# Performance work log

Hardware: AMD Instinct MI355X
Metric: run time of the kernel (lower is better)

## Reference

```python
import jax, jax.numpy as jnp
import numpy as np


def lstm_step(x_t, h, c, Wih, Whh, bih, bhh):
    # PyTorch LSTM gate order: i, f, g, o
    gates = x_t @ Wih.T + h @ Whh.T + bih + bhh
    i, f, g, o = jnp.split(gates, 4, axis=-1)
    i = jax.nn.sigmoid(i)
    f = jax.nn.sigmoid(f)
    g = jnp.tanh(g)
    o = jax.nn.sigmoid(o)
    c_new = f * c + i * g
    h_new = o * jnp.tanh(c_new)
    return h_new, c_new


def setup_inputs() -> dict:
    key = jax.random.key(0)
    N, C, T, V, M = 512, 3, 300, 25, 2
    F = C * V * M  # 150
    H = 100
    ks = jax.random.split(key, 12)
    s = 1.0 / np.sqrt(H)  # PyTorch LSTM/Linear init scale
    u = lambda k, shape: jax.random.uniform(k, shape, jnp.float32, -s, s)
    return {
        "x": jax.random.normal(ks[0], (N, C, T, V, M), jnp.float32),
        "enc_Wih": u(ks[1], (4 * H, F)),
        "enc_Whh": u(ks[2], (4 * H, H)),
        "enc_bih": u(ks[3], (4 * H,)),
        "enc_bhh": u(ks[4], (4 * H,)),
        "dec_Wih": u(ks[5], (4 * H, F)),
        "dec_Whh": u(ks[6], (4 * H, H)),
        "dec_bih": u(ks[7], (4 * H,)),
        "dec_bhh": u(ks[8], (4 * H,)),
        "fc_W": u(ks[9], (F, H)),
        "fc_b": u(ks[10], (F,)),
    }


def reference(x, enc_Wih, enc_Whh, enc_bih, enc_bhh,
              dec_Wih, dec_Whh, dec_bih, dec_bhh, fc_W, fc_b):
    N, C, T, V, M = x.shape
    F = C * V * M
    H = enc_Whh.shape[1]
    # (N,C,T,V,M) -> (N,T,C*V*M)
    xs = jnp.transpose(x, (0, 2, 1, 3, 4)).reshape(N, T, F)

    # Encoder LSTM: only need final (h, c)
    h0 = jnp.zeros((N, H), x.dtype)
    c0 = jnp.zeros((N, H), x.dtype)

    def enc_step(carry, xt):
        h, c = carry
        h, c = lstm_step(xt, h, c, enc_Wih, enc_Whh, enc_bih, enc_bhh)
        return (h, c), None

    (h, c), _ = jax.lax.scan(enc_step, (h0, c0), jnp.swapaxes(xs, 0, 1))

    inp0 = jnp.zeros((N, F), x.dtype)

    def dec_step(carry, _):
        inp, h, c = carry
        h, c = lstm_step(inp, h, c, dec_Wih, dec_Whh, dec_bih, dec_bhh)
        out = h @ fc_W.T + fc_b
        return (out, h, c), out

    _, outs = jax.lax.scan(dec_step, (inp0, h, c), None, length=T - 1)  # [T-1,N,F]

    # outputs[:,0,:] stays zero, like the torch.zeros buffer
    outputs = jnp.concatenate([jnp.zeros((1, N, F), x.dtype), outs], axis=0)  # [T,N,F]
    outputs = jnp.swapaxes(outputs, 0, 1).reshape(N, T, C, V, M)
    return jnp.transpose(outputs, (0, 2, 1, 3, 4))  # (N,C,T,V,M)
```

## Files before the change

### kernel.cpp

```cpp
#include <hip/hip_runtime.h>
#include <hip/hip_fp16.h>


#define B_W2P   0u
#define B_WDP   102400u
#define B_WEP   204800u
#define B_PIH   307200u
#define B_BENC  460800u
#define B_B1    462848u
#define B_BEFF  464896u
#define B_HIST  466944u
#define HIST_STRIDE 29952
#define B_XG    31137792u

typedef _Float16 h2_t __attribute__((ext_vector_type(2)));

#if defined(__has_builtin)
#if __has_builtin(__builtin_amdgcn_fdot2)
#define HAS_FDOT2 1
#endif
#endif

__device__ __forceinline__ float fdot2u(unsigned a, unsigned b, float c) {
#ifdef HAS_FDOT2
  return __builtin_amdgcn_fdot2(__builtin_bit_cast(h2_t, a), __builtin_bit_cast(h2_t, b), c, false);
#else
  float al = __half2float(__ushort_as_half((unsigned short)(a & 0xffffu)));
  float ah = __half2float(__ushort_as_half((unsigned short)(a >> 16)));
  float bl = __half2float(__ushort_as_half((unsigned short)(b & 0xffffu)));
  float bh = __half2float(__ushort_as_half((unsigned short)(b >> 16)));
  return fmaf(ah, bh, fmaf(al, bl, c));
#endif
}

__device__ __forceinline__ unsigned pack2f(float a, float b) {
  return (unsigned)__half_as_ushort(__float2half(a)) |
         ((unsigned)__half_as_ushort(__float2half(b)) << 16);
}

__device__ __forceinline__ float fast_sig(float x) {
  float e = __builtin_amdgcn_exp2f(x * -1.442695040888963f);
  return __builtin_amdgcn_rcpf(1.f + e);
}
__device__ __forceinline__ float fast_tanh(float x) {
  float e = __builtin_amdgcn_exp2f(x * -2.885390081777926f);
  return fmaf(2.f, __builtin_amdgcn_rcpf(1.f + e), -1.f);
}

__device__ __forceinline__ float lstm_tail(float acc, int ty, float& c) {
  float sg = fast_sig(acc);
  float th = fast_tanh(acc);
  float act = (ty == 2) ? th : sg;
  float v1 = __shfl_xor(act, 1);
  float v2 = __shfl_xor(act, 2);
  float v3 = __shfl_xor(v1, 2);
  c = fmaf(v1, c, act * v2);
  return v3 * fast_tanh(c);
}

__device__ __forceinline__ float dot100(const unsigned short* hb, const unsigned* wp) {
  const uint4* h4 = (const uint4*)hb;
  float a0 = 0.f, a1 = 0.f, a2 = 0.f, a3 = 0.f;
#pragma unroll
  for (int ch = 0; ch < 12; ++ch) {
    uint4 v = h4[ch];
    a0 = fdot2u(wp[4 * ch + 0], v.x, a0);
    a1 = fdot2u(wp[4 * ch + 1], v.y, a1);
    a2 = fdot2u(wp[4 * ch + 2], v.z, a2);
    a3 = fdot2u(wp[4 * ch + 3], v.w, a3);
  }
  uint2 v2 = *(const uint2*)(hb + 96);
  a0 = fdot2u(wp[48], v2.x, a0);
  a1 = fdot2u(wp[49], v2.y, a1);
  return (a0 + a1) + (a2 + a3);
}

__global__ void prep(const float* __restrict__ dWih, const float* __restrict__ dWhh,
                     const float* __restrict__ dbih, const float* __restrict__ dbhh,
                     const float* __restrict__ eWih, const float* __restrict__ eWhh,
                     const float* __restrict__ ebih, const float* __restrict__ ebhh,
                     const float* __restrict__ fcW,  const float* __restrict__ fcb,
                     char* __restrict__ wsb)
{
  int idx = blockIdx.x * 256 + threadIdx.x;
  if (idx < 25600) {
    int q = idx >> 9, t = idx & 511;
    unsigned w2p = 0, wdp = 0, wep = 0;
    if (t < 400) {
      int r = (t & 3) * 100 + (t >> 2);
      int j0 = 2 * q, j1 = 2 * q + 1;
      float wd0 = dWhh[r * 100 + j0], wd1 = dWhh[r * 100 + j1];
      float we0 = eWhh[r * 100 + j0], we1 = eWhh[r * 100 + j1];
      float s0 = 0.f, s1 = 0.f;
      for (int f = 0; f < 150; ++f) {
        float a = dWih[r * 150 + f];
        s0 = fmaf(a, fcW[f * 100 + j0], s0);
        s1 = fmaf(a, fcW[f * 100 + j1], s1);
      }
      w2p = pack2f(wd0 + s0, wd1 + s1);
      wdp = pack2f(wd0, wd1);
      wep = pack2f(we0, we1);
    }
    ((unsigned*)(wsb + B_W2P))[idx] = w2p;
    ((unsigned*)(wsb + B_WDP))[idx] = wdp;
    ((unsigned*)(wsb + B_WEP))[idx] = wep;
  } else if (idx < 25600 + 38400) {
    int k = idx - 25600; int d = k >> 9, t = k & 511;
    unsigned pk = 0;
    if (t < 400) {
      int r = (t & 3) * 100 + (t >> 2);
      pk = pack2f(eWih[r * 150 + 2 * d], eWih[r * 150 + 2 * d + 1]);
    }
    ((unsigned*)(wsb + B_PIH))[k] = pk;
  } else if (idx < 25600 + 38400 + 512) {
    int t = idx - (25600 + 38400);
    float be = 0.f, b1 = 0.f, bf = 0.f;
    if (t < 400) {
      int r = (t & 3) * 100 + (t >> 2);
      be = ebih[r] + ebhh[r];
      b1 = dbih[r] + dbhh[r];
      float acc = 0.f;
      for (int f = 0; f < 150; ++f) acc = fmaf(dWih[r * 150 + f], fcb[f], acc);
      bf = b1 + acc;
    }
    ((float*)(wsb + B_BENC))[t] = be;
    ((float*)(wsb + B_B1))[t]   = b1;
    ((float*)(wsb + B_BEFF))[t] = bf;
  }
}

__global__ __launch_bounds__(512, 4)
void pre(const float* __restrict__ x, const char* __restrict__ wsb,
         unsigned short* __restrict__ xg, int n0)
{
  const int tid = threadIdx.x;
  const int n = n0 + blockIdx.x;
  __shared__ unsigned short xls[150 * 160];

  unsigned wih[75];
  const unsigned* pih = (const unsigned*)(wsb + B_PIH);
#pragma unroll
  for (int d = 0; d < 75; ++d) wih[d] = pih[(d << 9) + tid];

  const float* xb = x + (size_t)n * 45000;
  unsigned short* xgr = xg + (size_t)blockIdx.x * 120000 + ((tid < 400) ? tid : 0);
  const bool on = tid < 400;

  for (int phase = 0; phase < 2; ++phase) {
    const int tbase = phase * 150;
    if (phase) __syncthreads();
    for (int d = tid; d < 150 * 160; d += 512) {
      int tl = d / 160, f = d - tl * 160;
      float v = 0.f;
      if (f < 150) {
        int c = f / 50, q = f - c * 50;
        v = xb[c * 15000 + (tbase + tl) * 50 + q];
      }
      xls[tl * 160 + f] = __half_as_ushort(__float2half(v));
    }
    __syncthreads();
    if (on) {
      for (int tl = 0; tl < 150; ++tl) {
        const uint4* row = (const uint4*)(xls + tl * 160);
        float a0 = 0.f, a1 = 0.f, a2 = 0.f, a3 = 0.f;
#pragma unroll
        for (int ch = 0; ch < 18; ++ch) {
          uint4 v = row[ch];
          a0 = fdot2u(wih[4 * ch + 0], v.x, a0);
          a1 = fdot2u(wih[4 * ch + 1], v.y, a1);
          a2 = fdot2u(wih[4 * ch + 2], v.z, a2);
          a3 = fdot2u(wih[4 * ch + 3], v.w, a3);
        }
        uint4 v = row[18];
        a0 = fdot2u(wih[72], v.x, a0);
        a1 = fdot2u(wih[73], v.y, a1);
        a2 = fdot2u(wih[74], v.z, a2);
        float a = (a0 + a1) + (a2 + a3);
        xgr[(size_t)(tbase + tl) * 400] = __half_as_ushort(__float2half(a));
      }
    }
  }
}

__global__ __launch_bounds__(512, 4)
void recurrent(const unsigned short* __restrict__ xg, char* __restrict__ wsb, int n0)
{
  const int t  = threadIdx.x;
  const int n  = n0 + blockIdx.x;
  const int j  = t >> 2, ty = t & 3;
  const bool leader = (t < 400) && (ty == 0);
  __shared__ unsigned short hh[2][112];

  const unsigned* WEP = (const unsigned*)(wsb + B_WEP);
  const unsigned* WDP = (const unsigned*)(wsb + B_WDP);
  const unsigned* W2P = (const unsigned*)(wsb + B_W2P);

  unsigned wp[50];
#pragma unroll
  for (int q = 0; q < 50; ++q) wp[q] = WEP[(q << 9) + t];

  const float benc = ((const float*)(wsb + B_BENC))[t];
  const float b1g  = ((const float*)(wsb + B_B1))[t];
  const float beff = ((const float*)(wsb + B_BEFF))[t];
  unsigned short* histn = (unsigned short*)(wsb + B_HIST) + (size_t)n * HIST_STRIDE;
  const unsigned short* xgr = xg + (size_t)blockIdx.x * 120000 + ((t < 400) ? t : 0);
  float c = 0.f;

  unsigned short p1 = xgr[400];
  {
    float acc = benc + __half2float(__ushort_as_half(xgr[0]));
    float hn = lstm_tail(acc, ty, c);
    if (leader) hh[1][j] = __half_as_ushort(__float2half(hn));
    __syncthreads();
  }
  for (int ts = 1; ts < 300; ++ts) {
    const int rd = ts & 1, wr = rd ^ 1;
    unsigned short pn = xgr[(size_t)((ts + 1 < 300) ? ts + 1 : 299) * 400];
    float acc = benc + __half2float(__ushort_as_half(p1)) + dot100(hh[rd], wp);
    float hn = lstm_tail(acc, ty, c);
    if (leader) hh[wr][j] = __half_as_ushort(__float2half(hn));
    __syncthreads();
    p1 = pn;
  }

#pragma unroll
  for (int q = 0; q < 50; ++q) wp[q] = WDP[(q << 9) + t];
  {
    float acc = b1g + dot100(hh[0], wp);
    float hn = lstm_tail(acc, ty, c);
    if (leader) {
      hh[1][j] = __half_as_ushort(__float2half(hn));
      histn[j] = __half_as_ushort(__float2half(hn));
    }
    __syncthreads();
  }
#pragma unroll
  for (int q = 0; q < 50; ++q) wp[q] = W2P[(q << 9) + t];
  for (int s = 2; s <= 299; ++s) {
    const int rd = (299 + s) & 1, wr = rd ^ 1;
    float acc = beff + dot100(hh[rd], wp);
    float hn = lstm_tail(acc, ty, c);
    if (leader) {
      hh[wr][j] = __half_as_ushort(__float2half(hn));
      histn[(s - 1) * 100 + j] = __half_as_ushort(__float2half(hn));
    }
    __syncthreads();
  }
}

__global__ __launch_bounds__(192, 4)
void emit(const char* __restrict__ wsb, const float* __restrict__ fcW,
          const float* __restrict__ fcb, float* __restrict__ out)
{
  const int f = threadIdx.x;
  const int n = blockIdx.x;
  const int z = blockIdx.y;
  __shared__ unsigned short hl[15008];

  const uint4* src = (const uint4*)((const unsigned short*)(wsb + B_HIST) +
                                    (size_t)n * HIST_STRIDE + z * 15000);
  for (int k = f; k < 1875; k += 192) ((uint4*)hl)[k] = src[k];

  const bool on = f < 150;
  unsigned fw[50];
  float bias = 0.f;
  if (on) {
    const float* fp = fcW + f * 100;
#pragma unroll
    for (int q = 0; q < 50; ++q) fw[q] = pack2f(fp[2 * q], fp[2 * q + 1]);
    bias = fcb[f];
  }
  __syncthreads();

  if (!on) return;
  const int cc = f / 50, r = f - cc * 50;
  float* ob = out + (size_t)n * 45000 + cc * 15000 + r;
  if (z == 0) ob[0] = 0.f;
  const int rows = z ? 149 : 150;
  for (int tl = 0; tl < rows; ++tl) {
    const uint4* row = (const uint4*)(hl + tl * 100);
    float a0 = bias, a1 = 0.f, a2 = 0.f, a3 = 0.f;
#pragma unroll
    for (int ch = 0; ch < 12; ++ch) {
      uint4 v = row[ch];
      a0 = fdot2u(fw[4 * ch + 0], v.x, a0);
      a1 = fdot2u(fw[4 * ch + 1], v.y, a1);
      a2 = fdot2u(fw[4 * ch + 2], v.z, a2);
      a3 = fdot2u(fw[4 * ch + 3], v.w, a3);
    }
    uint2 v2 = *(const uint2*)(hl + tl * 100 + 96);
    a0 = fdot2u(fw[48], v2.x, a0);
    a1 = fdot2u(fw[49], v2.y, a1);
    const int tt = z * 150 + tl + 1;
    ob[tt * 50] = (a0 + a1) + (a2 + a3);
  }
}

extern "C" void kernel_launch(void* const* d_in, const int* in_sizes, int n_in,
                              void* d_out, int out_size, void* d_ws, size_t ws_size,
                              hipStream_t stream) {
  const float* x    = (const float*)d_in[0];
  const float* eWih = (const float*)d_in[1];
  const float* eWhh = (const float*)d_in[2];
  const float* ebih = (const float*)d_in[3];
  const float* ebhh = (const float*)d_in[4];
  const float* dWih = (const float*)d_in[5];
  const float* dWhh = (const float*)d_in[6];
  const float* dbih = (const float*)d_in[7];
  const float* dbhh = (const float*)d_in[8];
  const float* fcW  = (const float*)d_in[9];
  const float* fcb  = (const float*)d_in[10];
  float* out = (float*)d_out;
  char* wsb  = (char*)d_ws;

  int npass = 1;
  while (npass < 8) {
    size_t need = (size_t)B_XG + (size_t)(512 / npass) * 300 * 400 * 2;
    if (need <= ws_size) break;
    npass *= 2;
  }
  const int chunk = 512 / npass;
  unsigned short* xg = (unsigned short*)(wsb + B_XG);

  prep<<<252, 256, 0, stream>>>(dWih, dWhh, dbih, dbhh, eWih, eWhh, ebih, ebhh, fcW, fcb, wsb);
  for (int p = 0; p < npass; ++p) {
    pre<<<chunk, 512, 0, stream>>>(x, wsb, xg, p * chunk);
    recurrent<<<chunk, 512, 0, stream>>>(xg, wsb, p * chunk);
  }
  emit<<<dim3(512, 2), 192, 0, stream>>>(wsb, fcW, fcb, out);
}
```

Baseline: 1.136 ms.

## Batch 16 sequences per block and run LSTM gate matmuls on MFMA

The recurrent kernel now handles 16 batch elements per block and computes the gate matmuls for all 16 with 16x16x32 fp16 MFMA instructions. Weight fragments are pre-laid-out by new prep kernels, replacing per-thread fdot2 dot products with per-sequence blocks. The input projection kernel also moves to MFMA over 16-sequence tiles, and the gate layout is rearranged so each lane holds all four gates and no cross-lane shuffles are needed. The cost is only 32 recurrent blocks, so few CUs are busy, with a 599-step serial chain per block.

```diff
diff --git a/kernel.cpp b/kernel.cpp
--- a/kernel.cpp
+++ b/kernel.cpp
@@ -2,19 +2,24 @@
 #include <hip/hip_fp16.h>
 
 
-#define B_W2P   0u
-#define B_WDP   102400u
-#define B_WEP   204800u
-#define B_PIH   307200u
-#define B_BENC  460800u
-#define B_B1    462848u
-#define B_BEFF  464896u
-#define B_HIST  466944u
+#define B_HIST   0u
 #define HIST_STRIDE 29952
-#define B_XG    31137792u
+#define B_W2S    30670848u
+#define B_BEFFS  30830848u
+#define B_AWIH   30832448u
+#define B_AENC   30975808u
+#define B_ADEC1  31090496u
+#define B_ADEC2  31205184u
+#define B_BENCF  31319872u
+#define B_B1F    31348544u
+#define B_BEFFF  31377216u
+#define B_XG     31405888u
+#define XG_PER_BG 4300800u
+
+typedef _Float16 f16x8 __attribute__((ext_vector_type(8)));
+typedef float    f32x4 __attribute__((ext_vector_type(4)));
 
 typedef _Float16 h2_t __attribute__((ext_vector_type(2)));
-
 #if defined(__has_builtin)
 #if __has_builtin(__builtin_amdgcn_fdot2)
 #define HAS_FDOT2 1
@@ -33,11 +38,13 @@
 #endif
 }
 
+__device__ __forceinline__ unsigned pkrtz(float a, float b) {
+  return __builtin_bit_cast(unsigned, __builtin_amdgcn_cvt_pkrtz(a, b));
+}
 __device__ __forceinline__ unsigned pack2f(float a, float b) {
   return (unsigned)__half_as_ushort(__float2half(a)) |
          ((unsigned)__half_as_ushort(__float2half(b)) << 16);
 }
-
 __device__ __forceinline__ float fast_sig(float x) {
   float e = __builtin_amdgcn_exp2f(x * -1.442695040888963f);
   return __builtin_amdgcn_rcpf(1.f + e);
@@ -46,205 +53,249 @@
   float e = __builtin_amdgcn_exp2f(x * -2.885390081777926f);
   return fmaf(2.f, __builtin_amdgcn_rcpf(1.f + e), -1.f);
 }
-
-__device__ __forceinline__ float lstm_tail(float acc, int ty, float& c) {
-  float sg = fast_sig(acc);
-  float th = fast_tanh(acc);
-  float act = (ty == 2) ? th : sg;
-  float v1 = __shfl_xor(act, 1);
-  float v2 = __shfl_xor(act, 2);
-  float v3 = __shfl_xor(v1, 2);
-  c = fmaf(v1, c, act * v2);
-  return v3 * fast_tanh(c);
-}
-
-__device__ __forceinline__ float dot100(const unsigned short* hb, const unsigned* wp) {
-  const uint4* h4 = (const uint4*)hb;
-  float a0 = 0.f, a1 = 0.f, a2 = 0.f, a3 = 0.f;
-#pragma unroll
-  for (int ch = 0; ch < 12; ++ch) {
-    uint4 v = h4[ch];
-    a0 = fdot2u(wp[4 * ch + 0], v.x, a0);
-    a1 = fdot2u(wp[4 * ch + 1], v.y, a1);
-    a2 = fdot2u(wp[4 * ch + 2], v.z, a2);
-    a3 = fdot2u(wp[4 * ch + 3], v.w, a3);
-  }
-  uint2 v2 = *(const uint2*)(hb + 96);
-  a0 = fdot2u(wp[48], v2.x, a0);
-  a1 = fdot2u(wp[49], v2.y, a1);
-  return (a0 + a1) + (a2 + a3);
-}
-
-__global__ void prep(const float* __restrict__ dWih, const float* __restrict__ dWhh,
-                     const float* __restrict__ dbih, const float* __restrict__ dbhh,
-                     const float* __restrict__ eWih, const float* __restrict__ eWhh,
-                     const float* __restrict__ ebih, const float* __restrict__ ebhh,
-                     const float* __restrict__ fcW,  const float* __restrict__ fcb,
-                     char* __restrict__ wsb)
+__device__ __forceinline__ f32x4 mfma16(uint4 a, uint4 b, f32x4 c) {
+  return __builtin_amdgcn_mfma_f32_16x16x32_f16(
+      __builtin_bit_cast(f16x8, a), __builtin_bit_cast(f16x8, b), c, 0, 0, 0);
+}
+__device__ __forceinline__ float uslo(unsigned u) {
+  return __half2float(__ushort_as_half((unsigned short)(u & 0xffffu)));
+}
+__device__ __forceinline__ float ushi(unsigned u) {
+  return __half2float(__ushort_as_half((unsigned short)(u >> 16)));
+}
+
+__global__ void prep_w2(const float* __restrict__ dWih, const float* __restrict__ dWhh,
+                        const float* __restrict__ dbih, const float* __restrict__ dbhh,
+                        const float* __restrict__ fcW,  const float* __restrict__ fcb,
+                        char* __restrict__ wsb)
 {
   int idx = blockIdx.x * 256 + threadIdx.x;
-  if (idx < 25600) {
-    int q = idx >> 9, t = idx & 511;
-    unsigned w2p = 0, wdp = 0, wep = 0;
-    if (t < 400) {
-      int r = (t & 3) * 100 + (t >> 2);
-      int j0 = 2 * q, j1 = 2 * q + 1;
-      float wd0 = dWhh[r * 100 + j0], wd1 = dWhh[r * 100 + j1];
-      float we0 = eWhh[r * 100 + j0], we1 = eWhh[r * 100 + j1];
-      float s0 = 0.f, s1 = 0.f;
-      for (int f = 0; f < 150; ++f) {
-        float a = dWih[r * 150 + f];
-        s0 = fmaf(a, fcW[f * 100 + j0], s0);
-        s1 = fmaf(a, fcW[f * 100 + j1], s1);
+  if (idx < 40000) {
+    int r = idx / 100, j = idx - r * 100;
+    float s = 0.f;
+    for (int f = 0; f < 150; ++f) s = fmaf(dWih[r * 150 + f], fcW[f * 100 + j], s);
+    ((float*)(wsb + B_W2S))[idx] = dWhh[r * 100 + j] + s;
+  } else if (idx < 40400) {
+    int r = idx - 40000;
+    float s = 0.f;
+    for (int f = 0; f < 150; ++f) s = fmaf(dWih[r * 150 + f], fcb[f], s);
+    ((float*)(wsb + B_BEFFS))[r] = dbih[r] + dbhh[r] + s;
+  }
+}
+
+__global__ void prep_frags(const float* __restrict__ eWih, const float* __restrict__ eWhh,
+                           const float* __restrict__ dWhh,
+                           const float* __restrict__ ebih, const float* __restrict__ ebhh,
+                           const float* __restrict__ dbih, const float* __restrict__ dbhh,
+                           char* __restrict__ wsb)
+{
+  int idx = blockIdx.x * 256 + threadIdx.x;
+  const float* w2s = (const float*)(wsb + B_W2S);
+  const float* beffs = (const float*)(wsb + B_BEFFS);
+  if (idx < 8960) {
+    int l = idx & 63, fi = idx >> 6;
+    int kc = fi % 5, mt = fi / 5;
+    int w = mt >> 2, ty = mt & 3;
+    int gr = w * 16 + (l & 15);
+    int r = ty * 100 + gr;
+    int k0 = kc * 32 + (l >> 4) * 8;
+    unsigned u[4];
+    for (int p = 0; p < 4; ++p) {
+      int k = k0 + 2 * p;
+      float v0 = (gr < 100 && k     < 150) ? eWih[r * 150 + k]     : 0.f;
+      float v1 = (gr < 100 && k + 1 < 150) ? eWih[r * 150 + k + 1] : 0.f;
+      u[p] = pack2f(v0, v1);
+    }
+    ((uint4*)(wsb + B_AWIH))[idx] = make_uint4(u[0], u[1], u[2], u[3]);
+  } else if (idx < 8960 + 3 * 7168) {
+    int t = idx - 8960;
+    int set = t / 7168, q = t - set * 7168;
+    int l = q & 63, fi = q >> 6;
+    int kc = fi & 3, mt = fi >> 2;
+    int w = mt >> 2, ty = mt & 3;
+    int gr = w * 16 + (l & 15);
+    int r = ty * 100 + gr;
+    int k0 = kc * 32 + (l >> 4) * 8;
+    unsigned u[4];
+    for (int p = 0; p < 4; ++p) {
+      int k = k0 + 2 * p;
+      float v0 = 0.f, v1 = 0.f;
+      if (gr < 100) {
+        if (k < 100)     v0 = set == 0 ? eWhh[r*100+k]   : set == 1 ? dWhh[r*100+k]   : w2s[r*100+k];
+        if (k + 1 < 100) v1 = set == 0 ? eWhh[r*100+k+1] : set == 1 ? dWhh[r*100+k+1] : w2s[r*100+k+1];
       }
-      w2p = pack2f(wd0 + s0, wd1 + s1);
-      wdp = pack2f(wd0, wd1);
-      wep = pack2f(we0, we1);
-    }
-    ((unsigned*)(wsb + B_W2P))[idx] = w2p;
-    ((unsigned*)(wsb + B_WDP))[idx] = wdp;
-    ((unsigned*)(wsb + B_WEP))[idx] = wep;
-  } else if (idx < 25600 + 38400) {
-    int k = idx - 25600; int d = k >> 9, t = k & 511;
-    unsigned pk = 0;
-    if (t < 400) {
-      int r = (t & 3) * 100 + (t >> 2);
-      pk = pack2f(eWih[r * 150 + 2 * d], eWih[r * 150 + 2 * d + 1]);
-    }
-    ((unsigned*)(wsb + B_PIH))[k] = pk;
-  } else if (idx < 25600 + 38400 + 512) {
-    int t = idx - (25600 + 38400);
-    float be = 0.f, b1 = 0.f, bf = 0.f;
-    if (t < 400) {
-      int r = (t & 3) * 100 + (t >> 2);
-      be = ebih[r] + ebhh[r];
-      b1 = dbih[r] + dbhh[r];
-      float acc = 0.f;
-      for (int f = 0; f < 150; ++f) acc = fmaf(dWih[r * 150 + f], fcb[f], acc);
-      bf = b1 + acc;
-    }
-    ((float*)(wsb + B_BENC))[t] = be;
-    ((float*)(wsb + B_B1))[t]   = b1;
-    ((float*)(wsb + B_BEFF))[t] = bf;
-  }
-}
-
-__global__ __launch_bounds__(512, 4)
-void pre(const float* __restrict__ x, const char* __restrict__ wsb,
-         unsigned short* __restrict__ xg, int n0)
+      u[p] = pack2f(v0, v1);
+    }
+    ((uint4*)(wsb + B_AENC + (unsigned)set * 114688u))[q] = make_uint4(u[0], u[1], u[2], u[3]);
+  } else if (idx < 8960 + 21504 + 3 * 1792) {
+    int t = idx - 8960 - 21504;
+    int set = t / 1792, q = t - set * 1792;
+    int l = q & 63, mt = q >> 6;
+    int w = mt >> 2, ty = mt & 3;
+    float v[4];
+    for (int rr = 0; rr < 4; ++rr) {
+      int gr = w * 16 + (l >> 4) * 4 + rr;
+      int r = ty * 100 + gr;
+      v[rr] = 0.f;
+      if (gr < 100)
+        v[rr] = set == 0 ? ebih[r] + ebhh[r] : set == 1 ? dbih[r] + dbhh[r] : beffs[r];
+    }
+    ((float4*)(wsb + B_BENCF + (unsigned)set * 28672u))[q] = make_float4(v[0], v[1], v[2], v[3]);
+  }
+}
+
+__global__ __launch_bounds__(64)
+void pre(const float* __restrict__ x, char* __restrict__ wsb, int nbase)
+{
+  const int l = threadIdx.x;
+  const int tg = blockIdx.x;
+  const int b  = blockIdx.y;
+  const int quad = l >> 4, nn = l & 15;
+  __shared__ unsigned short xls[4][16][168];
+
+  const int t0 = tg * 4;
+  const int n0 = nbase + b * 16;
+  for (int it = 0; it < 84; ++it) {
+    int i = l + it * 64;
+    int tp = i / 1344; int rem = i - tp * 1344;
+    int np = rem / 84; int p = rem - np * 84;
+    unsigned val = 0;
+    if (p < 75) {
+      int f0 = 2 * p; int c = f0 / 50; int q = f0 - c * 50;
+      const float2 v = *(const float2*)(x + (size_t)(n0 + np) * 45000 + c * 15000 + (t0 + tp) * 50 + q);
+      val = pkrtz(v.x, v.y);
+    }
+    *(unsigned*)&xls[tp][np][2 * p] = val;
+  }
+  __syncthreads();
+
+  uint4 B[4][5];
+#pragma unroll
+  for (int u = 0; u < 4; ++u)
+#pragma unroll
+    for (int kc = 0; kc < 5; ++kc)
+      B[u][kc] = *(const uint4*)&xls[u][nn][kc * 32 + quad * 8];
+
+  const uint4* awih = (const uint4*)(wsb + B_AWIH);
+  const float4* bencf = (const float4*)(wsb + B_BENCF);
+  unsigned short* xgo = (unsigned short*)(wsb + B_XG);
+
+  for (int mt = 0; mt < 28; ++mt) {
+    const int w = mt >> 2, ty = mt & 3;
+    uint4 A0 = awih[(mt * 5 + 0) * 64 + l];
+    uint4 A1 = awih[(mt * 5 + 1) * 64 + l];
+    uint4 A2 = awih[(mt * 5 + 2) * 64 + l];
+    uint4 A3 = awih[(mt * 5 + 3) * 64 + l];
+    uint4 A4 = awih[(mt * 5 + 4) * 64 + l];
+    float4 bi = bencf[mt * 64 + l];
+    f32x4 bias; bias[0] = bi.x; bias[1] = bi.y; bias[2] = bi.z; bias[3] = bi.w;
+#pragma unroll
+    for (int u = 0; u < 4; ++u) {
+      f32x4 acc = bias;
+      acc = mfma16(A0, B[u][0], acc);
+      acc = mfma16(A1, B[u][1], acc);
+      acc = mfma16(A2, B[u][2], acc);
+      acc = mfma16(A3, B[u][3], acc);
+      acc = mfma16(A4, B[u][4], acc);
+      unsigned u0 = pkrtz(acc[0], acc[1]);
+      unsigned u1 = pkrtz(acc[2], acc[3]);
+      size_t off = ((size_t)(b * 300 + t0 + u) * 7 + w) * 1024 + l * 16 + ty * 4;
+      *(uint2*)(xgo + off) = make_uint2(u0, u1);
+    }
+  }
+}
+
+__global__ __launch_bounds__(448)
+void recurrent(char* __restrict__ wsb, int nbase)
 {
   const int tid = threadIdx.x;
-  const int n = n0 + blockIdx.x;
-  __shared__ unsigned short xls[150 * 160];
-
-  unsigned wih[75];
-  const unsigned* pih = (const unsigned*)(wsb + B_PIH);
-#pragma unroll
-  for (int d = 0; d < 75; ++d) wih[d] = pih[(d << 9) + tid];
-
-  const float* xb = x + (size_t)n * 45000;
-  unsigned short* xgr = xg + (size_t)blockIdx.x * 120000 + ((tid < 400) ? tid : 0);
-  const bool on = tid < 400;
-
-  for (int phase = 0; phase < 2; ++phase) {
-    const int tbase = phase * 150;
-    if (phase) __syncthreads();
-    for (int d = tid; d < 150 * 160; d += 512) {
-      int tl = d / 160, f = d - tl * 160;
-      float v = 0.f;
-      if (f < 150) {
-        int c = f / 50, q = f - c * 50;
-        v = xb[c * 15000 + (tbase + tl) * 50 + q];
+  const int l = tid & 63, w = tid >> 6;
+  const int quad = l >> 4, n = l & 15;
+  const int c0 = w * 16 + quad * 4;
+  __shared__ unsigned short hbuf[2][16][136];
+
+  for (int i = tid; i < 2176; i += 448) ((unsigned*)hbuf)[i] = 0;
+
+  const uint4* aenc  = (const uint4*)(wsb + B_AENC);
+  const uint4* adec1 = (const uint4*)(wsb + B_ADEC1);
+  const uint4* adec2 = (const uint4*)(wsb + B_ADEC2);
+  uint4 A[4][4];
+#pragma unroll
+  for (int ty = 0; ty < 4; ++ty)
+#pragma unroll
+    for (int kc = 0; kc < 4; ++kc)
+      A[ty][kc] = aenc[((w * 4 + ty) * 4 + kc) * 64 + l];
+
+  f32x4 bias[4];
+  float cst[4] = {0.f, 0.f, 0.f, 0.f};
+
+  const uint4* xgw = (const uint4*)(wsb + B_XG) + (size_t)blockIdx.x * 300 * 896 + (w * 64 + l) * 2;
+  uint4 xa = xgw[0], xb = xgw[1];
+
+  unsigned short* hist = (unsigned short*)(wsb + B_HIST) +
+                         (size_t)(nbase + blockIdx.x * 16 + n) * HIST_STRIDE + c0;
+  const bool hist_on = (c0 < 100);
+
+  for (int g = 0; g < 599; ++g) {
+    __syncthreads();
+    const int rd = g & 1, wr = rd ^ 1;
+    uint4 B0 = *(const uint4*)&hbuf[rd][n][0  + quad * 8];
+    uint4 B1 = *(const uint4*)&hbuf[rd][n][32 + quad * 8];
+    uint4 B2 = *(const uint4*)&hbuf[rd][n][64 + quad * 8];
+    uint4 B3 = *(const uint4*)&hbuf[rd][n][96 + quad * 8];
+
+    f32x4 acc[4];
+    if (g < 300) {
+      acc[0][0] = uslo(xa.x); acc[0][1] = ushi(xa.x); acc[0][2] = uslo(xa.y); acc[0][3] = ushi(xa.y);
+      acc[1][0] = uslo(xa.z); acc[1][1] = ushi(xa.z); acc[1][2] = uslo(xa.w); acc[1][3] = ushi(xa.w);
+      acc[2][0] = uslo(xb.x); acc[2][1] = ushi(xb.x); acc[2][2] = uslo(xb.y); acc[2][3] = ushi(xb.y);
+      acc[3][0] = uslo(xb.z); acc[3][1] = ushi(xb.z); acc[3][2] = uslo(xb.w); acc[3][3] = ushi(xb.w);
+      if (g < 299) { const uint4* p = xgw + (size_t)(g + 1) * 896; xa = p[0]; xb = p[1]; }
+    } else {
+#pragma unroll
+      for (int ty = 0; ty < 4; ++ty) acc[ty] = bias[ty];
+    }
+
+#pragma unroll
+    for (int kc = 0; kc < 4; ++kc) {
+      uint4 Bk = (kc == 0) ? B0 : (kc == 1) ? B1 : (kc == 2) ? B2 : B3;
+#pragma unroll
+      for (int ty = 0; ty < 4; ++ty) acc[ty] = mfma16(A[ty][kc], Bk, acc[ty]);
+    }
+
+    float hv[4];
+#pragma unroll
+    for (int r = 0; r < 4; ++r) {
+      float si = fast_sig(acc[0][r]);
+      float sf = fast_sig(acc[1][r]);
+      float tg = fast_tanh(acc[2][r]);
+      float so = fast_sig(acc[3][r]);
+      cst[r] = fmaf(sf, cst[r], si * tg);
+      hv[r] = so * fast_tanh(cst[r]);
+    }
+    unsigned u0 = pkrtz(hv[0], hv[1]);
+    unsigned u1 = pkrtz(hv[2], hv[3]);
+    *(uint2*)&hbuf[wr][n][c0] = make_uint2(u0, u1);
+    if (g >= 300 && hist_on)
+      *(uint2*)(hist + (size_t)(g - 300) * 100) = make_uint2(u0, u1);
+
+    if (g == 299) {
+#pragma unroll
+      for (int ty = 0; ty < 4; ++ty) {
+#pragma unroll
+        for (int kc = 0; kc < 4; ++kc) A[ty][kc] = adec1[((w * 4 + ty) * 4 + kc) * 64 + l];
+        float4 bv = ((const float4*)(wsb + B_B1F))[(w * 4 + ty) * 64 + l];
+        bias[ty][0] = bv.x; bias[ty][1] = bv.y; bias[ty][2] = bv.z; bias[ty][3] = bv.w;
       }
-      xls[tl * 160 + f] = __half_as_ushort(__float2half(v));
-    }
-    __syncthreads();
-    if (on) {
-      for (int tl = 0; tl < 150; ++tl) {
-        const uint4* row = (const uint4*)(xls + tl * 160);
-        float a0 = 0.f, a1 = 0.f, a2 = 0.f, a3 = 0.f;
-#pragma unroll
-        for (int ch = 0; ch < 18; ++ch) {
-          uint4 v = row[ch];
-          a0 = fdot2u(wih[4 * ch + 0], v.x, a0);
-          a1 = fdot2u(wih[4 * ch + 1], v.y, a1);
-          a2 = fdot2u(wih[4 * ch + 2], v.z, a2);
-          a3 = fdot2u(wih[4 * ch + 3], v.w, a3);
-        }
-        uint4 v = row[18];
-        a0 = fdot2u(wih[72], v.x, a0);
-        a1 = fdot2u(wih[73], v.y, a1);
-        a2 = fdot2u(wih[74], v.z, a2);
-        float a = (a0 + a1) + (a2 + a3);
-        xgr[(size_t)(tbase + tl) * 400] = __half_as_ushort(__float2half(a));
+    } else if (g == 300) {
+#pragma unroll
+      for (int ty = 0; ty < 4; ++ty) {
+#pragma unroll
+        for (int kc = 0; kc < 4; ++kc) A[ty][kc] = adec2[((w * 4 + ty) * 4 + kc) * 64 + l];
+        float4 bv = ((const float4*)(wsb + B_BEFFF))[(w * 4 + ty) * 64 + l];
+        bias[ty][0] = bv.x; bias[ty][1] = bv.y; bias[ty][2] = bv.z; bias[ty][3] = bv.w;
       }
     }
-  }
-}
-
-__global__ __launch_bounds__(512, 4)
-void recurrent(const unsigned short* __restrict__ xg, char* __restrict__ wsb, int n0)
-{
-  const int t  = threadIdx.x;
-  const int n  = n0 + blockIdx.x;
-  const int j  = t >> 2, ty = t & 3;
-  const bool leader = (t < 400) && (ty == 0);
-  __shared__ unsigned short hh[2][112];
-
-  const unsigned* WEP = (const unsigned*)(wsb + B_WEP);
-  const unsigned* WDP = (const unsigned*)(wsb + B_WDP);
-  const unsigned* W2P = (const unsigned*)(wsb + B_W2P);
-
-  unsigned wp[50];
-#pragma unroll
-  for (int q = 0; q < 50; ++q) wp[q] = WEP[(q << 9) + t];
-
-  const float benc = ((const float*)(wsb + B_BENC))[t];
-  const float b1g  = ((const float*)(wsb + B_B1))[t];
-  const float beff = ((const float*)(wsb + B_BEFF))[t];
-  unsigned short* histn = (unsigned short*)(wsb + B_HIST) + (size_t)n * HIST_STRIDE;
-  const unsigned short* xgr = xg + (size_t)blockIdx.x * 120000 + ((t < 400) ? t : 0);
-  float c = 0.f;
-
-  unsigned short p1 = xgr[400];
-  {
-    float acc = benc + __half2float(__ushort_as_half(xgr[0]));
-    float hn = lstm_tail(acc, ty, c);
-    if (leader) hh[1][j] = __half_as_ushort(__float2half(hn));
-    __syncthreads();
-  }
-  for (int ts = 1; ts < 300; ++ts) {
-    const int rd = ts & 1, wr = rd ^ 1;
-    unsigned short pn = xgr[(size_t)((ts + 1 < 300) ? ts + 1 : 299) * 400];
-    float acc = benc + __half2float(__ushort_as_half(p1)) + dot100(hh[rd], wp);
-    float hn = lstm_tail(acc, ty, c);
-    if (leader) hh[wr][j] = __half_as_ushort(__float2half(hn));
-    __syncthreads();
-    p1 = pn;
-  }
-
-#pragma unroll
-  for (int q = 0; q < 50; ++q) wp[q] = WDP[(q << 9) + t];
-  {
-    float acc = b1g + dot100(hh[0], wp);
-    float hn = lstm_tail(acc, ty, c);
-    if (leader) {
-      hh[1][j] = __half_as_ushort(__float2half(hn));
-      histn[j] = __half_as_ushort(__float2half(hn));
-    }
-    __syncthreads();
-  }
-#pragma unroll
-  for (int q = 0; q < 50; ++q) wp[q] = W2P[(q << 9) + t];
-  for (int s = 2; s <= 299; ++s) {
-    const int rd = (299 + s) & 1, wr = rd ^ 1;
-    float acc = beff + dot100(hh[rd], wp);
-    float hn = lstm_tail(acc, ty, c);
-    if (leader) {
-      hh[wr][j] = __half_as_ushort(__float2half(hn));
-      histn[(s - 1) * 100 + j] = __half_as_ushort(__float2half(hn));
-    }
-    __syncthreads();
   }
 }
 
@@ -263,12 +314,12 @@
 
   const bool on = f < 150;
   unsigned fw[50];
-  float bias = 0.f;
+  float biasv = 0.f;
   if (on) {
     const float* fp = fcW + f * 100;
 #pragma unroll
     for (int q = 0; q < 50; ++q) fw[q] = pack2f(fp[2 * q], fp[2 * q + 1]);
-    bias = fcb[f];
+    biasv = fcb[f];
   }
   __syncthreads();
 
@@ -279,7 +330,7 @@
   const int rows = z ? 149 : 150;
   for (int tl = 0; tl < rows; ++tl) {
     const uint4* row = (const uint4*)(hl + tl * 100);
-    float a0 = bias, a1 = 0.f, a2 = 0.f, a3 = 0.f;
+    float a0 = biasv, a1 = 0.f, a2 = 0.f, a3 = 0.f;
 #pragma unroll
     for (int ch = 0; ch < 12; ++ch) {
       uint4 v = row[ch];
@@ -314,18 +365,17 @@
   char* wsb  = (char*)d_ws;
 
   int npass = 1;
-  while (npass < 8) {
-    size_t need = (size_t)B_XG + (size_t)(512 / npass) * 300 * 400 * 2;
-    if (need <= ws_size) break;
+  while (npass < 32) {
+    if ((size_t)B_XG + (size_t)(32 / npass) * XG_PER_BG <= ws_size) break;
     npass *= 2;
   }
-  const int chunk = 512 / npass;
-  unsigned short* xg = (unsigned short*)(wsb + B_XG);
-
-  prep<<<252, 256, 0, stream>>>(dWih, dWhh, dbih, dbhh, eWih, eWhh, ebih, ebhh, fcW, fcb, wsb);
+  const int bg = 32 / npass;
+
+  prep_w2<<<158, 256, 0, stream>>>(dWih, dWhh, dbih, dbhh, fcW, fcb, wsb);
+  prep_frags<<<140, 256, 0, stream>>>(eWih, eWhh, dWhh, ebih, ebhh, dbih, dbhh, wsb);
   for (int p = 0; p < npass; ++p) {
-    pre<<<chunk, 512, 0, stream>>>(x, wsb, xg, p * chunk);
-    recurrent<<<chunk, 512, 0, stream>>>(xg, wsb, p * chunk);
+    pre<<<dim3(75, bg), 64, 0, stream>>>(x, wsb, p * bg * 16);
+    recurrent<<<bg, 448, 0, stream>>>(wsb, p * bg * 16);
   }
   emit<<<dim3(512, 2), 192, 0, stream>>>(wsb, fcW, fcb, out);
 }
```

Result: slower. 1.407 ms (+23.9%).
